# Performance work log

Measured on AMD Instinct MI355X. Metric: run time of the kernel, lower is better.

The kernel has to match this reference:

```python
import jax, jax.numpy as jnp
import numpy as np

N = 10000      # nodes
E = 320000     # edges
IN_DIM = 256
HID = 256
EDGE_DIM = 64


def _sage(x, src, dst, w_l, b_l, w_r, n_nodes):
    """PyG SAGEConv (aggr='mean', root_weight=True, normalize=False):
    out_i = lin_l(mean_{j->i} x_j) + lin_r(x_i). Messages flow src->dst."""
    msg = x[src]                                            # [E, F]
    agg = jax.ops.segment_sum(msg, dst, num_segments=n_nodes)
    cnt = jax.ops.segment_sum(jnp.ones((msg.shape[0], 1), x.dtype), dst,
                              num_segments=n_nodes)
    mean = agg / jnp.maximum(cnt, 1.0)                      # [N, F]
    return mean @ w_l.T + b_l + x @ w_r.T                   # [N, HID]


def setup_inputs() -> dict:
    key = jax.random.key(0)
    ks = jax.random.split(key, 13)
    s = 0.02
    return {
        "x": jax.random.normal(ks[0], (N, IN_DIM), dtype=jnp.float32),
        "edge_attr": jax.random.normal(ks[1], (E, EDGE_DIM), dtype=jnp.float32),
        "conv1_wl": jax.random.normal(ks[2], (HID, IN_DIM), dtype=jnp.float32) * s,
        "conv1_bl": jnp.zeros((HID,), dtype=jnp.float32),
        "conv1_wr": jax.random.normal(ks[3], (HID, IN_DIM), dtype=jnp.float32) * s,
        "conv2_wl": jax.random.normal(ks[4], (HID, HID), dtype=jnp.float32) * s,
        "conv2_bl": jnp.zeros((HID,), dtype=jnp.float32),
        "conv2_wr": jax.random.normal(ks[5], (HID, HID), dtype=jnp.float32) * s,
        "mlp_w1": jax.random.normal(ks[6], (HID, 2 * HID + EDGE_DIM), dtype=jnp.float32) * s,
        "mlp_b1": jnp.zeros((HID,), dtype=jnp.float32),
        "mlp_w2": jax.random.normal(ks[7], (1, HID), dtype=jnp.float32) * s,
        "mlp_b2": jnp.zeros((1,), dtype=jnp.float32),
        "edge_index": jax.random.randint(ks[8], (2, E), 0, N, dtype=jnp.int32),
    }


def reference(x, edge_attr, conv1_wl, conv1_bl, conv1_wr,
              conv2_wl, conv2_bl, conv2_wr,
              mlp_w1, mlp_b1, mlp_w2, mlp_b2, edge_index):
    src, dst = edge_index[0], edge_index[1]
    # encode_nodes (dropout is identity in eval mode)
    h = jax.nn.relu(_sage(x, src, dst, conv1_wl, conv1_bl, conv1_wr, N))
    h = _sage(h, src, dst, conv2_wl, conv2_bl, conv2_wr, N)
    # edge_logits: gather endpoints, concat with edge_attr, 2-layer MLP
    feats = jnp.concatenate([h[src], h[dst], edge_attr], axis=1)   # [E, 2H+ED]
    hidden = jax.nn.relu(feats @ mlp_w1.T + mlp_b1)                # [E, H]
    logits = hidden @ mlp_w2.T + mlp_b2                            # [E, 1]
    return logits[:, 0]
```

## Files before the change

### kernel.cpp

```cpp
#include <hip/hip_runtime.h>

#define N_NODES 10000
#define N_EDGES 320000
#define DIM 256
#define ED 64
#define W1_LD 576

__global__ void hist_kernel(const int* __restrict__ dst, int* __restrict__ cnt, int n) {
  int i = blockIdx.x * blockDim.x + threadIdx.x;
  if (i < n) atomicAdd(&cnt[dst[i]], 1);
}

__global__ void scan_kernel(const int* __restrict__ cnt, int* __restrict__ off,
                            int* __restrict__ cursor, int n) {
  __shared__ int wsum[4];
  __shared__ int carry_s;
  int t = threadIdx.x, lane = t & 63, w = t >> 6;
  if (t == 0) carry_s = 0;
  __syncthreads();
  for (int base = 0; base < n; base += 256) {
    int i = base + t;
    int v = (i < n) ? cnt[i] : 0;
    int sc = v;
    #pragma unroll
    for (int s = 1; s < 64; s <<= 1) {
      int u = __shfl_up(sc, s, 64);
      if (lane >= s) sc += u;
    }
    if (lane == 63) wsum[w] = sc;
    __syncthreads();
    int woff = 0, tot = 0;
    #pragma unroll
    for (int j = 0; j < 4; ++j) { int s = wsum[j]; if (j < w) woff += s; tot += s; }
    int excl = sc - v + woff + carry_s;
    if (i < n) { off[i] = excl; cursor[i] = excl; }
    __syncthreads();
    if (t == 0) carry_s += tot;
    __syncthreads();
  }
  if (t == 0) off[n] = carry_s;
}

__global__ void scatter_kernel(const int* __restrict__ src, const int* __restrict__ dst,
                               int* __restrict__ cursor, int* __restrict__ csr_src,
                               int* __restrict__ csr_dst, int* __restrict__ csr_eid, int n) {
  int i = blockIdx.x * blockDim.x + threadIdx.x;
  if (i < n) {
    int d = dst[i];
    int p = atomicAdd(&cursor[d], 1);
    csr_src[p] = src[i];
    csr_dst[p] = d;
    csr_eid[p] = i;
  }
}

__global__ __launch_bounds__(256) void aggregate_kernel(
    const float* __restrict__ X, const int* __restrict__ off,
    const int* __restrict__ csr_src, float* __restrict__ out) {
  int node = blockIdx.x * 4 + (threadIdx.x >> 6);
  int t4 = (threadIdx.x & 63) * 4;
  int beg = off[node], end = off[node + 1];
  float x0=0.f,y0=0.f,z0=0.f,w0=0.f, x1=0.f,y1=0.f,z1=0.f,w1=0.f;
  float x2=0.f,y2=0.f,z2=0.f,w2=0.f, x3=0.f,y3=0.f,z3=0.f,w3=0.f;
  int e = beg;
  for (; e + 3 < end; e += 4) {
    int s0 = csr_src[e], s1 = csr_src[e+1], s2 = csr_src[e+2], s3 = csr_src[e+3];
    float4 v0 = *(const float4*)&X[(size_t)s0 * DIM + t4];
    float4 v1 = *(const float4*)&X[(size_t)s1 * DIM + t4];
    float4 v2 = *(const float4*)&X[(size_t)s2 * DIM + t4];
    float4 v3 = *(const float4*)&X[(size_t)s3 * DIM + t4];
    x0+=v0.x; y0+=v0.y; z0+=v0.z; w0+=v0.w;
    x1+=v1.x; y1+=v1.y; z1+=v1.z; w1+=v1.w;
    x2+=v2.x; y2+=v2.y; z2+=v2.z; w2+=v2.w;
    x3+=v3.x; y3+=v3.y; z3+=v3.z; w3+=v3.w;
  }
  for (; e < end; ++e) {
    int s = csr_src[e];
    float4 v = *(const float4*)&X[(size_t)s * DIM + t4];
    x0+=v.x; y0+=v.y; z0+=v.z; w0+=v.w;
  }
  int deg = end - beg;
  float inv = 1.0f / (float)(deg > 0 ? deg : 1);
  float4 r;
  r.x = (x0+x1+x2+x3) * inv; r.y = (y0+y1+y2+y3) * inv;
  r.z = (z0+z1+z2+z3) * inv; r.w = (w0+w1+w2+w3) * inv;
  *(float4*)&out[(size_t)node * DIM + t4] = r;
}

template<bool SECOND, bool RELU>
__global__ __launch_bounds__(256) void gemm_kernel(
    const float* __restrict__ W1_, const float* __restrict__ A1,
    const float* __restrict__ A2, const float* __restrict__ W2_,
    const float* __restrict__ bias, float* __restrict__ C,
    int nrows, int K, int ldw, int ldc, int wsplit) {
  __shared__ float As[32][64];
  __shared__ float Bs[32][64];
  int t = threadIdx.x;
  int tx = t & 15, ty = t >> 4;
  int row0 = blockIdx.x * 64;
  int col0 = blockIdx.y * 64;

  const float* W1 = W1_;
  const float* W2 = W2_;
  bool qreg = (col0 >= wsplit);
  if (qreg) {
    ptrdiff_t adj = (ptrdiff_t)wsplit - (ptrdiff_t)wsplit * (ptrdiff_t)ldw;
    W1 = W1_ + adj; W2 = W2_ + adj;
  }

  float acc[4][4];
  #pragma unroll
  for (int i = 0; i < 4; ++i)
    #pragma unroll
    for (int j = 0; j < 4; ++j) acc[i][j] = 0.f;

  int ksteps = K / 32;
  int total = SECOND ? 2 * ksteps : ksteps;
  for (int kt = 0; kt < total; ++kt) {
    bool second = SECOND && (kt >= ksteps);
    const float* A = second ? A2 : A1;
    const float* W = second ? W2 : W1;
    int kb = (second ? (kt - ksteps) : kt) * 32;
    __syncthreads();
    #pragma unroll
    for (int i = 0; i < 2; ++i) {
      int idx = i * 256 + t;
      int m = idx >> 3;
      int kq = idx & 7;
      int row = row0 + m;
      float4 v = make_float4(0.f, 0.f, 0.f, 0.f);
      if (row < nrows) v = *(const float4*)&A[(size_t)row * K + kb + kq * 4];
      As[kq * 4 + 0][m] = v.x; As[kq * 4 + 1][m] = v.y;
      As[kq * 4 + 2][m] = v.z; As[kq * 4 + 3][m] = v.w;
    }
    #pragma unroll
    for (int i = 0; i < 2; ++i) {
      int idx = i * 256 + t;
      int o = idx >> 3;
      int kq = idx & 7;
      float4 v = *(const float4*)&W[(size_t)(col0 + o) * ldw + kb + kq * 4];
      Bs[kq * 4 + 0][o] = v.x; Bs[kq * 4 + 1][o] = v.y;
      Bs[kq * 4 + 2][o] = v.z; Bs[kq * 4 + 3][o] = v.w;
    }
    __syncthreads();
    #pragma unroll 8
    for (int k = 0; k < 32; ++k) {
      float4 a0 = *(const float4*)&As[k][ty * 4];
      float4 b0 = *(const float4*)&Bs[k][tx * 4];
      float a[4] = {a0.x, a0.y, a0.z, a0.w};
      float b[4] = {b0.x, b0.y, b0.z, b0.w};
      #pragma unroll
      for (int i = 0; i < 4; ++i)
        #pragma unroll
        for (int j = 0; j < 4; ++j)
          acc[i][j] += a[i] * b[j];
    }
  }
  float4 bv = make_float4(0.f, 0.f, 0.f, 0.f);
  if (bias && !qreg) bv = *(const float4*)&bias[col0 + tx * 4];
  #pragma unroll
  for (int i = 0; i < 4; ++i) {
    int row = row0 + ty * 4 + i;
    if (row < nrows) {
      float4 o4;
      o4.x = acc[i][0] + bv.x; o4.y = acc[i][1] + bv.y;
      o4.z = acc[i][2] + bv.z; o4.w = acc[i][3] + bv.w;
      if (RELU) {
        o4.x = fmaxf(o4.x, 0.f); o4.y = fmaxf(o4.y, 0.f);
        o4.z = fmaxf(o4.z, 0.f); o4.w = fmaxf(o4.w, 0.f);
      }
      *(float4*)&C[(size_t)row * ldc + col0 + tx * 4] = o4;
    }
  }
}

#define EB 64
__global__ __launch_bounds__(256, 4) void edge_kernel(
    const float* __restrict__ edge_attr,
    const int* __restrict__ csr_src, const int* __restrict__ csr_dst,
    const int* __restrict__ csr_eid,
    const float* __restrict__ PQ,
    const float* __restrict__ mlp_w1,
    const float* __restrict__ w2,
    const float* __restrict__ b2,
    float* __restrict__ out) {
  __shared__ float w_lds[64][64];
  __shared__ float ea_lds[64][EB];

  int t = threadIdx.x;
  int e0 = blockIdx.x * EB;
  {
    int e_l = t >> 2, q = t & 3;
    int eid = csr_eid[e0 + e_l];
    const float* ep = &edge_attr[(size_t)eid * ED + q * 16];
    #pragma unroll
    for (int j = 0; j < 4; ++j) {
      float4 v = *(const float4*)&ep[j * 4];
      int k = q * 16 + j * 4;
      ea_lds[k + 0][e_l] = v.x; ea_lds[k + 1][e_l] = v.y;
      ea_lds[k + 2][e_l] = v.z; ea_lds[k + 3][e_l] = v.w;
    }
  }
  int c = t & 15, r = t >> 4;
  const float* pbase[4];
  const float* qbase[4];
  int eout[4];
  #pragma unroll
  for (int i = 0; i < 4; ++i) {
    int el = e0 + r * 4 + i;
    pbase[i] = &PQ[(size_t)csr_src[el] * 512 + c * 4];
    qbase[i] = &PQ[(size_t)csr_dst[el] * 512 + 256 + c * 4];
    eout[i] = csr_eid[el];
  }
  float logit[4] = {0.f, 0.f, 0.f, 0.f};
  float4 pf[4], qf[4];
  #pragma unroll
  for (int i = 0; i < 4; ++i) {
    pf[i] = *(const float4*)&pbase[i][0];
    qf[i] = *(const float4*)&qbase[i][0];
  }

  for (int chunk = 0; chunk < 4; ++chunk) {
    #pragma unroll
    for (int i = 0; i < 4; ++i) {
      int idx = i * 256 + t;
      int o = idx & 63;
      int kq = idx >> 6;
      float4 v = *(const float4*)&mlp_w1[(size_t)(chunk * 64 + o) * W1_LD + 512 + kq * 4];
      w_lds[kq * 4 + 0][o] = v.x; w_lds[kq * 4 + 1][o] = v.y;
      w_lds[kq * 4 + 2][o] = v.z; w_lds[kq * 4 + 3][o] = v.w;
    }
    __syncthreads();
    float acc[4][4];
    #pragma unroll
    for (int i = 0; i < 4; ++i)
      #pragma unroll
      for (int j = 0; j < 4; ++j) acc[i][j] = 0.f;
    #pragma unroll 8
    for (int k = 0; k < 64; ++k) {
      float4 a = *(const float4*)&ea_lds[k][r * 4];
      float4 wv4 = *(const float4*)&w_lds[k][c * 4];
      float av[4] = {a.x, a.y, a.z, a.w};
      float wv[4] = {wv4.x, wv4.y, wv4.z, wv4.w};
      #pragma unroll
      for (int i = 0; i < 4; ++i)
        #pragma unroll
        for (int j = 0; j < 4; ++j)
          acc[i][j] += av[i] * wv[j];
    }
    float4 w2v = *(const float4*)&w2[chunk * 64 + c * 4];
    #pragma unroll
    for (int i = 0; i < 4; ++i) {
      float s0 = fmaxf(acc[i][0] + pf[i].x + qf[i].x, 0.f);
      float s1 = fmaxf(acc[i][1] + pf[i].y + qf[i].y, 0.f);
      float s2 = fmaxf(acc[i][2] + pf[i].z + qf[i].z, 0.f);
      float s3 = fmaxf(acc[i][3] + pf[i].w + qf[i].w, 0.f);
      logit[i] += s0 * w2v.x + s1 * w2v.y + s2 * w2v.z + s3 * w2v.w;
    }
    if (chunk < 3) {
      int coff = (chunk + 1) * 64;
      #pragma unroll
      for (int i = 0; i < 4; ++i) {
        pf[i] = *(const float4*)&pbase[i][coff];
        qf[i] = *(const float4*)&qbase[i][coff];
      }
      __syncthreads();
    }
  }
  #pragma unroll
  for (int m = 1; m < 16; m <<= 1) {
    #pragma unroll
    for (int i = 0; i < 4; ++i) logit[i] += __shfl_xor(logit[i], m, 64);
  }
  if (c == 0) {
    float bb = b2[0];
    #pragma unroll
    for (int i = 0; i < 4; ++i) out[eout[i]] = logit[i] + bb;
  }
}

static inline size_t alignup(size_t x) { return (x + 255) & ~(size_t)255; }

extern "C" void kernel_launch(void* const* d_in, const int* in_sizes, int n_in,
                              void* d_out, int out_size, void* d_ws, size_t ws_size,
                              hipStream_t stream) {
  const float* x    = (const float*)d_in[0];
  const float* ea   = (const float*)d_in[1];
  const float* c1wl = (const float*)d_in[2];
  const float* c1bl = (const float*)d_in[3];
  const float* c1wr = (const float*)d_in[4];
  const float* c2wl = (const float*)d_in[5];
  const float* c2bl = (const float*)d_in[6];
  const float* c2wr = (const float*)d_in[7];
  const float* w1   = (const float*)d_in[8];
  const float* b1   = (const float*)d_in[9];
  const float* w2   = (const float*)d_in[10];
  const float* b2   = (const float*)d_in[11];
  const int*   ei   = (const int*)d_in[12];
  const int* src = ei;
  const int* dst = ei + N_EDGES;
  float* out = (float*)d_out;

  char* p = (char*)d_ws;
  size_t o = 0;
  int* cnt      = (int*)(p + o); o += alignup(N_NODES * 4);
  int* off      = (int*)(p + o); o += alignup((N_NODES + 1) * 4);
  int* cursor   = (int*)(p + o); o += alignup(N_NODES * 4);
  int* csr_src  = (int*)(p + o); o += alignup(N_EDGES * 4);
  int* csr_dst  = (int*)(p + o); o += alignup(N_EDGES * 4);
  int* csr_eid  = (int*)(p + o); o += alignup(N_EDGES * 4);
  float* mbuf   = (float*)(p + o); o += alignup((size_t)N_NODES * DIM * 4);
  float* h1     = (float*)(p + o); o += alignup((size_t)N_NODES * DIM * 4);
  float* h2     = (float*)(p + o); o += alignup((size_t)N_NODES * DIM * 4);
  float* PQ     = (float*)(p + o); o += alignup((size_t)N_NODES * 512 * 4);

  hipMemsetAsync(cnt, 0, N_NODES * 4, stream);
  hist_kernel<<<(N_EDGES + 255) / 256, 256, 0, stream>>>(dst, cnt, N_EDGES);
  scan_kernel<<<1, 256, 0, stream>>>(cnt, off, cursor, N_NODES);
  scatter_kernel<<<(N_EDGES + 255) / 256, 256, 0, stream>>>(
      src, dst, cursor, csr_src, csr_dst, csr_eid, N_EDGES);

  dim3 ggrid((N_NODES + 63) / 64, 4);
  dim3 pqgrid((N_NODES + 63) / 64, 8);
  const int NOSPLIT = 1 << 30;

  aggregate_kernel<<<N_NODES / 4, 256, 0, stream>>>(x, off, csr_src, mbuf);
  gemm_kernel<true, true><<<ggrid, 256, 0, stream>>>(
      c1wl, mbuf, x, c1wr, c1bl, h1, N_NODES, DIM, DIM, DIM, NOSPLIT);

  aggregate_kernel<<<N_NODES / 4, 256, 0, stream>>>(h1, off, csr_src, mbuf);
  gemm_kernel<true, false><<<ggrid, 256, 0, stream>>>(
      c2wl, mbuf, h1, c2wr, c2bl, h2, N_NODES, DIM, DIM, DIM, NOSPLIT);

  gemm_kernel<false, false><<<pqgrid, 256, 0, stream>>>(
      w1, h2, h2, w1, b1, PQ, N_NODES, DIM, W1_LD, 512, 256);

  edge_kernel<<<N_EDGES / EB, 256, 0, stream>>>(
      ea, csr_src, csr_dst, csr_eid, PQ, w1, w2, b2, out);
}
```

Baseline: 616.4 us.

## Transform-then-aggregate SAGE layers and enlarge edge kernel blocks

Each SAGE layer now runs the linear projections first (x·Wl and x·Wr into one 512-wide buffer) and then does a fused mean-aggregation kernel. That kernel adds the root term and the bias and applies ReLU, which removes the separate mean buffer and the two-input GEMM. The gather loop is unrolled to 8 neighbors. The edge kernel moves to 128-edge, 512-thread blocks. Gathers now read rows with a 512-float stride, and the edge kernel's register and LDS pressure changes with the larger blocks.

```diff
diff --git a/kernel.cpp b/kernel.cpp
--- a/kernel.cpp
+++ b/kernel.cpp
@@ -54,45 +54,59 @@
   }
 }
 
-__global__ __launch_bounds__(256) void aggregate_kernel(
-    const float* __restrict__ X, const int* __restrict__ off,
-    const int* __restrict__ csr_src, float* __restrict__ out) {
+template<bool RELU>
+__global__ __launch_bounds__(256) void agg_fused_kernel(
+    const float* __restrict__ XP,
+    const int* __restrict__ off, const int* __restrict__ csr_src,
+    const float* __restrict__ bias,
+    float* __restrict__ H) {
   int node = blockIdx.x * 4 + (threadIdx.x >> 6);
   int t4 = (threadIdx.x & 63) * 4;
   int beg = off[node], end = off[node + 1];
-  float x0=0.f,y0=0.f,z0=0.f,w0=0.f, x1=0.f,y1=0.f,z1=0.f,w1=0.f;
-  float x2=0.f,y2=0.f,z2=0.f,w2=0.f, x3=0.f,y3=0.f,z3=0.f,w3=0.f;
+  float4 root = *(const float4*)&XP[(size_t)node * 512 + 256 + t4];
+  float4 bv = *(const float4*)&bias[t4];
+  float sx = 0.f, sy = 0.f, sz = 0.f, sw = 0.f;
   int e = beg;
-  for (; e + 3 < end; e += 4) {
-    int s0 = csr_src[e], s1 = csr_src[e+1], s2 = csr_src[e+2], s3 = csr_src[e+3];
-    float4 v0 = *(const float4*)&X[(size_t)s0 * DIM + t4];
-    float4 v1 = *(const float4*)&X[(size_t)s1 * DIM + t4];
-    float4 v2 = *(const float4*)&X[(size_t)s2 * DIM + t4];
-    float4 v3 = *(const float4*)&X[(size_t)s3 * DIM + t4];
-    x0+=v0.x; y0+=v0.y; z0+=v0.z; w0+=v0.w;
-    x1+=v1.x; y1+=v1.y; z1+=v1.z; w1+=v1.w;
-    x2+=v2.x; y2+=v2.y; z2+=v2.z; w2+=v2.w;
-    x3+=v3.x; y3+=v3.y; z3+=v3.z; w3+=v3.w;
+  for (; e + 7 < end; e += 8) {
+    int i0 = csr_src[e],   i1 = csr_src[e+1], i2 = csr_src[e+2], i3 = csr_src[e+3];
+    int i4 = csr_src[e+4], i5 = csr_src[e+5], i6 = csr_src[e+6], i7 = csr_src[e+7];
+    float4 v0 = *(const float4*)&XP[(size_t)i0 * 512 + t4];
+    float4 v1 = *(const float4*)&XP[(size_t)i1 * 512 + t4];
+    float4 v2 = *(const float4*)&XP[(size_t)i2 * 512 + t4];
+    float4 v3 = *(const float4*)&XP[(size_t)i3 * 512 + t4];
+    float4 v4 = *(const float4*)&XP[(size_t)i4 * 512 + t4];
+    float4 v5 = *(const float4*)&XP[(size_t)i5 * 512 + t4];
+    float4 v6 = *(const float4*)&XP[(size_t)i6 * 512 + t4];
+    float4 v7 = *(const float4*)&XP[(size_t)i7 * 512 + t4];
+    sx += ((v0.x + v1.x) + (v2.x + v3.x)) + ((v4.x + v5.x) + (v6.x + v7.x));
+    sy += ((v0.y + v1.y) + (v2.y + v3.y)) + ((v4.y + v5.y) + (v6.y + v7.y));
+    sz += ((v0.z + v1.z) + (v2.z + v3.z)) + ((v4.z + v5.z) + (v6.z + v7.z));
+    sw += ((v0.w + v1.w) + (v2.w + v3.w)) + ((v4.w + v5.w) + (v6.w + v7.w));
   }
   for (; e < end; ++e) {
     int s = csr_src[e];
-    float4 v = *(const float4*)&X[(size_t)s * DIM + t4];
-    x0+=v.x; y0+=v.y; z0+=v.z; w0+=v.w;
+    float4 v = *(const float4*)&XP[(size_t)s * 512 + t4];
+    sx += v.x; sy += v.y; sz += v.z; sw += v.w;
   }
   int deg = end - beg;
   float inv = 1.0f / (float)(deg > 0 ? deg : 1);
   float4 r;
-  r.x = (x0+x1+x2+x3) * inv; r.y = (y0+y1+y2+y3) * inv;
-  r.z = (z0+z1+z2+z3) * inv; r.w = (w0+w1+w2+w3) * inv;
-  *(float4*)&out[(size_t)node * DIM + t4] = r;
-}
-
-template<bool SECOND, bool RELU>
+  r.x = sx * inv + bv.x + root.x;
+  r.y = sy * inv + bv.y + root.y;
+  r.z = sz * inv + bv.z + root.z;
+  r.w = sw * inv + bv.w + root.w;
+  if (RELU) {
+    r.x = fmaxf(r.x, 0.f); r.y = fmaxf(r.y, 0.f);
+    r.z = fmaxf(r.z, 0.f); r.w = fmaxf(r.w, 0.f);
+  }
+  *(float4*)&H[(size_t)node * 256 + t4] = r;
+}
+
 __global__ __launch_bounds__(256) void gemm_kernel(
-    const float* __restrict__ W1_, const float* __restrict__ A1,
-    const float* __restrict__ A2, const float* __restrict__ W2_,
+    const float* __restrict__ A,
+    const float* __restrict__ Wlo, const float* __restrict__ Whi,
     const float* __restrict__ bias, float* __restrict__ C,
-    int nrows, int K, int ldw, int ldc, int wsplit) {
+    int nrows, int ldw, int split) {
   __shared__ float As[32][64];
   __shared__ float Bs[32][64];
   int t = threadIdx.x;
@@ -100,13 +114,9 @@
   int row0 = blockIdx.x * 64;
   int col0 = blockIdx.y * 64;
 
-  const float* W1 = W1_;
-  const float* W2 = W2_;
-  bool qreg = (col0 >= wsplit);
-  if (qreg) {
-    ptrdiff_t adj = (ptrdiff_t)wsplit - (ptrdiff_t)wsplit * (ptrdiff_t)ldw;
-    W1 = W1_ + adj; W2 = W2_ + adj;
-  }
+  const float* W = Wlo;
+  int obase = col0;
+  if (col0 >= split) { W = Whi; obase = col0 - split; }
 
   float acc[4][4];
   #pragma unroll
@@ -114,13 +124,8 @@
     #pragma unroll
     for (int j = 0; j < 4; ++j) acc[i][j] = 0.f;
 
-  int ksteps = K / 32;
-  int total = SECOND ? 2 * ksteps : ksteps;
-  for (int kt = 0; kt < total; ++kt) {
-    bool second = SECOND && (kt >= ksteps);
-    const float* A = second ? A2 : A1;
-    const float* W = second ? W2 : W1;
-    int kb = (second ? (kt - ksteps) : kt) * 32;
+  for (int kt = 0; kt < 8; ++kt) {
+    int kb = kt * 32;
     __syncthreads();
     #pragma unroll
     for (int i = 0; i < 2; ++i) {
@@ -129,7 +134,7 @@
       int kq = idx & 7;
       int row = row0 + m;
       float4 v = make_float4(0.f, 0.f, 0.f, 0.f);
-      if (row < nrows) v = *(const float4*)&A[(size_t)row * K + kb + kq * 4];
+      if (row < nrows) v = *(const float4*)&A[(size_t)row * 256 + kb + kq * 4];
       As[kq * 4 + 0][m] = v.x; As[kq * 4 + 1][m] = v.y;
       As[kq * 4 + 2][m] = v.z; As[kq * 4 + 3][m] = v.w;
     }
@@ -138,7 +143,7 @@
       int idx = i * 256 + t;
       int o = idx >> 3;
       int kq = idx & 7;
-      float4 v = *(const float4*)&W[(size_t)(col0 + o) * ldw + kb + kq * 4];
+      float4 v = *(const float4*)&W[(size_t)(obase + o) * ldw + kb + kq * 4];
       Bs[kq * 4 + 0][o] = v.x; Bs[kq * 4 + 1][o] = v.y;
       Bs[kq * 4 + 2][o] = v.z; Bs[kq * 4 + 3][o] = v.w;
     }
@@ -157,7 +162,7 @@
     }
   }
   float4 bv = make_float4(0.f, 0.f, 0.f, 0.f);
-  if (bias && !qreg) bv = *(const float4*)&bias[col0 + tx * 4];
+  if (bias && col0 < split) bv = *(const float4*)&bias[col0 + tx * 4];
   #pragma unroll
   for (int i = 0; i < 4; ++i) {
     int row = row0 + ty * 4 + i;
@@ -165,17 +170,13 @@
       float4 o4;
       o4.x = acc[i][0] + bv.x; o4.y = acc[i][1] + bv.y;
       o4.z = acc[i][2] + bv.z; o4.w = acc[i][3] + bv.w;
-      if (RELU) {
-        o4.x = fmaxf(o4.x, 0.f); o4.y = fmaxf(o4.y, 0.f);
-        o4.z = fmaxf(o4.z, 0.f); o4.w = fmaxf(o4.w, 0.f);
-      }
-      *(float4*)&C[(size_t)row * ldc + col0 + tx * 4] = o4;
-    }
-  }
-}
-
-#define EB 64
-__global__ __launch_bounds__(256, 4) void edge_kernel(
+      *(float4*)&C[(size_t)row * 512 + col0 + tx * 4] = o4;
+    }
+  }
+}
+
+#define EB 128
+__global__ __launch_bounds__(512, 6) void edge_kernel(
     const float* __restrict__ edge_attr,
     const int* __restrict__ csr_src, const int* __restrict__ csr_dst,
     const int* __restrict__ csr_eid,
@@ -222,8 +223,8 @@
 
   for (int chunk = 0; chunk < 4; ++chunk) {
     #pragma unroll
-    for (int i = 0; i < 4; ++i) {
-      int idx = i * 256 + t;
+    for (int i = 0; i < 2; ++i) {
+      int idx = i * 512 + t;
       int o = idx & 63;
       int kq = idx >> 6;
       float4 v = *(const float4*)&mlp_w1[(size_t)(chunk * 64 + o) * W1_LD + 512 + kq * 4];
@@ -309,9 +310,8 @@
   int* csr_src  = (int*)(p + o); o += alignup(N_EDGES * 4);
   int* csr_dst  = (int*)(p + o); o += alignup(N_EDGES * 4);
   int* csr_eid  = (int*)(p + o); o += alignup(N_EDGES * 4);
-  float* mbuf   = (float*)(p + o); o += alignup((size_t)N_NODES * DIM * 4);
-  float* h1     = (float*)(p + o); o += alignup((size_t)N_NODES * DIM * 4);
-  float* h2     = (float*)(p + o); o += alignup((size_t)N_NODES * DIM * 4);
+  float* XP     = (float*)(p + o); o += alignup((size_t)N_NODES * 512 * 4);
+  float* h      = (float*)(p + o); o += alignup((size_t)N_NODES * 256 * 4);
   float* PQ     = (float*)(p + o); o += alignup((size_t)N_NODES * 512 * 4);
 
   hipMemsetAsync(cnt, 0, N_NODES * 4, stream);
@@ -320,21 +320,16 @@
   scatter_kernel<<<(N_EDGES + 255) / 256, 256, 0, stream>>>(
       src, dst, cursor, csr_src, csr_dst, csr_eid, N_EDGES);
 
-  dim3 ggrid((N_NODES + 63) / 64, 4);
-  dim3 pqgrid((N_NODES + 63) / 64, 8);
-  const int NOSPLIT = 1 << 30;
-
-  aggregate_kernel<<<N_NODES / 4, 256, 0, stream>>>(x, off, csr_src, mbuf);
-  gemm_kernel<true, true><<<ggrid, 256, 0, stream>>>(
-      c1wl, mbuf, x, c1wr, c1bl, h1, N_NODES, DIM, DIM, DIM, NOSPLIT);
-
-  aggregate_kernel<<<N_NODES / 4, 256, 0, stream>>>(h1, off, csr_src, mbuf);
-  gemm_kernel<true, false><<<ggrid, 256, 0, stream>>>(
-      c2wl, mbuf, h1, c2wr, c2bl, h2, N_NODES, DIM, DIM, DIM, NOSPLIT);
-
-  gemm_kernel<false, false><<<pqgrid, 256, 0, stream>>>(
-      w1, h2, h2, w1, b1, PQ, N_NODES, DIM, W1_LD, 512, 256);
-
-  edge_kernel<<<N_EDGES / EB, 256, 0, stream>>>(
+  dim3 ggrid((N_NODES + 63) / 64, 8);
+
+  gemm_kernel<<<ggrid, 256, 0, stream>>>(x, c1wl, c1wr, nullptr, XP, N_NODES, DIM, 256);
+  agg_fused_kernel<true><<<N_NODES / 4, 256, 0, stream>>>(XP, off, csr_src, c1bl, h);
+
+  gemm_kernel<<<ggrid, 256, 0, stream>>>(h, c2wl, c2wr, nullptr, XP, N_NODES, DIM, 256);
+  agg_fused_kernel<false><<<N_NODES / 4, 256, 0, stream>>>(XP, off, csr_src, c2bl, h);
+
+  gemm_kernel<<<ggrid, 256, 0, stream>>>(h, w1, w1 + 256, b1, PQ, N_NODES, W1_LD, 256);
+
+  edge_kernel<<<N_EDGES / EB, 512, 0, stream>>>(
       ea, csr_src, csr_dst, csr_eid, PQ, w1, w2, b2, out);
 }
```

Result: slower. 678.3 us (+10.1%).
